# Optimization experiments

Hardware: AMD Instinct MI355X
Metric: run time of the kernel (lower is better)

## Reference

```python
import jax, jax.numpy as jnp
import numpy as np

B, C_IN, C_OUT, T, HID = 8, 32, 32, 8192, 64


def setup_inputs() -> dict:
    key = jax.random.key(0)
    ks = jax.random.split(key, 8)
    s1 = 1.0  # fan_in=1
    s2 = 1.0 / np.sqrt(HID)
    return {
        "x": jax.random.normal(ks[0], (B, C_IN, T), dtype=jnp.float32),
        "w1": jax.random.uniform(ks[1], (1, HID), jnp.float32, -s1, s1),
        "b1": jax.random.uniform(ks[2], (HID,), jnp.float32, -s1, s1),
        "w2": jax.random.uniform(ks[3], (HID, HID), jnp.float32, -s2, s2),
        "b2": jax.random.uniform(ks[4], (HID,), jnp.float32, -s2, s2),
        "w3": jax.random.uniform(ks[5], (HID, C_IN * C_OUT), jnp.float32, -s2, s2),
        "b3": jax.random.uniform(ks[6], (C_IN * C_OUT,), jnp.float32, -s2, s2),
        "bias": jnp.zeros((C_OUT,), dtype=jnp.float32),
    }


def _filters(w1, b1, w2, b2, w3, b3):
    # positions: (T, 1) in [0, 1]
    pos = jnp.linspace(0.0, 1.0, T, dtype=jnp.float32)[:, None]
    h = jax.nn.gelu(pos @ w1 + b1, approximate=False)
    h = jax.nn.gelu(h @ w2 + b2, approximate=False)
    f = h @ w3 + b3                      # (T, out*in)
    f = f.reshape(T, C_OUT, C_IN)
    return jnp.transpose(f, (1, 2, 0))   # (out, in, T)


def reference(x, w1, b1, w2, b2, w3, b3, bias):
    freq_x = jnp.fft.rfft(x, axis=-1)                      # (B, in, F)
    filt = _filters(w1, b1, w2, b2, w3, b3)                # (out, in, T)
    freq_f = jnp.fft.rfft(filt, axis=-1)                   # (out, in, F)
    conv_freq = jnp.einsum('bif,oif->bof', freq_x, freq_f) # contract over in
    out = jnp.fft.irfft(conv_freq, n=T, axis=-1)           # (B, out, T)
    return out + bias[None, :, None]
```

## Files before the change

### kernel.cpp

```cpp
#include <hip/hip_runtime.h>
#include <math.h>

#define T 8192
#define M 4096
#define JS 4104
#define B 8
#define CIN 32
#define COUT 32
#define HID 64
#define FT 4

__device__ inline float2 cadd(float2 a, float2 b){ return make_float2(a.x+b.x, a.y+b.y); }
__device__ inline float2 csub(float2 a, float2 b){ return make_float2(a.x-b.x, a.y-b.y); }
__device__ inline float2 cmul(float2 a, float2 b){ return make_float2(a.x*b.x - a.y*b.y, a.x*b.y + a.y*b.x); }
__device__ inline float2 cmulc(float2 a, float2 b){
    return make_float2(a.x*b.x + a.y*b.y, a.y*b.x - a.x*b.y); }
__device__ inline int swz(int p){ return p ^ ((p >> 5) & 31); }
__device__ inline int brev12(int v){ return (int)(__brev((unsigned)v) >> 20); }

__device__ inline float gelu_exact(float x){
    return 0.5f*x*(1.0f + erff(x*0.70710678118654752440f));
}

template<int S, int SH0>
__device__ inline void dif_group8(float2 q[8], int r, const float2* __restrict__ tw){
    #pragma unroll
    for (int st = 0; st < 3; ++st){
        const int d = 4 >> st;
        const int sh = SH0 + st;
        #pragma unroll
        for (int k = 0; k < 4; ++k){
            const int jd = k & (d-1);
            const int lo = ((k & ~(d-1)) << 1) | jd;
            const int hi = lo + d;
            float2 w = tw[(r + S*jd) << sh];
            float2 a = q[lo], b = q[hi];
            q[lo] = cadd(a, b);
            q[hi] = cmul(csub(a, b), w);
        }
    }
}
template<int S, int SH0>
__device__ inline void dit_group8(float2 q[8], int r, const float2* __restrict__ tw){
    #pragma unroll
    for (int st = 0; st < 3; ++st){
        const int d = 1 << st;
        const int sh = SH0 - st;
        #pragma unroll
        for (int k = 0; k < 4; ++k){
            const int jd = k & (d-1);
            const int lo = ((k & ~(d-1)) << 1) | jd;
            const int hi = lo + d;
            float2 w = tw[(r + S*jd) << sh];
            float2 a = q[lo];
            float2 t2 = cmulc(q[hi], w);
            q[lo] = cadd(a, t2);
            q[hi] = csub(a, t2);
        }
    }
}

__device__ inline void lds_store8(float2* sc, const float2* q, int base, int S){
    #pragma unroll
    for (int l = 0; l < 8; ++l) sc[swz(base + S*l)] = q[l];
}
__device__ inline void lds_load8(const float2* sc, float2* q, int base, int S){
    #pragma unroll
    for (int l = 0; l < 8; ++l) q[l] = sc[swz(base + S*l)];
}

__global__ __launch_bounds__(512) void rfft_all(const float* __restrict__ x,
        const float* __restrict__ H, const float2* __restrict__ tw,
        float2* __restrict__ Xh, float2* __restrict__ Hh){
    __shared__ float2 sc[M];
    const int t = threadIdx.x;
    const int sig = blockIdx.x;
    const float* srow;
    float2* dp;
    if (sig < B*CIN){ srow = x + (size_t)sig*T;        dp = Xh + (size_t)sig*JS; }
    else            { srow = H + (size_t)(sig-B*CIN)*T; dp = Hh + (size_t)(sig-B*CIN)*JS; }
    const float2* zp = (const float2*)srow;
    float2 q[8];
    #pragma unroll
    for (int l = 0; l < 8; ++l) q[l] = zp[t + 512*l];
    dif_group8<512,1>(q, t, tw);
    lds_store8(sc, q, t, 512);
    __syncthreads();
    {
        const int base = ((t>>6)<<9) | (t&63);
        lds_load8(sc, q, base, 64);
        dif_group8<64,4>(q, t&63, tw);
        lds_store8(sc, q, base, 64);
    }
    {
        const int base = ((t>>3)<<6) | (t&7);
        lds_load8(sc, q, base, 8);
        dif_group8<8,7>(q, t&7, tw);
        lds_store8(sc, q, base, 8);
    }
    {
        const int base = t << 3;
        lds_load8(sc, q, base, 1);
        dif_group8<1,10>(q, 0, tw);
        lds_store8(sc, q, base, 1);
    }
    __syncthreads();
    #pragma unroll
    for (int l = 0; l < 8; ++l){
        const int j  = t + 512*l;
        const int k  = brev12(j);
        const int j2 = brev12((M - k) & (M-1));
        float2 Z  = sc[swz(j)];
        float2 Zm = sc[swz(j2)];
        float2 E = make_float2(0.5f*(Z.x + Zm.x), 0.5f*(Z.y - Zm.y));
        float2 D = make_float2(Z.x - Zm.x, Z.y + Zm.y);
        float2 O = make_float2(0.5f*D.y, -0.5f*D.x);
        dp[j] = cadd(E, cmul(tw[k], O));
        if (j == 0) dp[M] = make_float2(Z.x - Z.y, 0.0f);
    }
}

__global__ __launch_bounds__(512) void irfft_out(const float2* __restrict__ Yh,
        const float2* __restrict__ tw, const float* __restrict__ bias, float* __restrict__ out){
    __shared__ float2 sc[M];
    const int t = threadIdx.x;
    const int sig = blockIdx.x;
    const float2* yp = Yh + (size_t)sig*JS;
    #pragma unroll
    for (int l = 0; l < 8; ++l){
        const int j = t + 512*l;
        sc[swz(j)] = yp[j];
    }
    float2 yM = yp[M];
    __syncthreads();
    #pragma unroll
    for (int l = 0; l < 4; ++l){
        const int j = (t + 512*l) << 1;
        const int k = brev12(j);
        float2 Ym; int j2 = 0;
        if (k == 0){ Ym = yM; }
        else { j2 = brev12(M - k); Ym = sc[swz(j2)]; }
        float2 Y = sc[swz(j)];
        float2 E = make_float2(0.5f*(Y.x + Ym.x), 0.5f*(Y.y - Ym.y));
        float2 D = make_float2(0.5f*(Y.x - Ym.x), 0.5f*(Y.y + Ym.y));
        float2 O = cmulc(D, tw[k]);
        sc[swz(j)] = make_float2(E.x - O.y, E.y + O.x);
        if (k != 0){
            sc[swz(j2)] = make_float2(E.x + O.y, O.x - E.y);
        }
    }
    if (t == 0){
        float2 Y = sc[swz(1)];
        float2 E = make_float2(Y.x, 0.0f);
        float2 D = make_float2(0.0f, Y.y);
        float2 O = cmulc(D, tw[2048]);
        sc[swz(1)] = make_float2(E.x - O.y, E.y + O.x);
    }
    __syncthreads();
    float2 q[8];
    {
        const int base = t << 3;
        lds_load8(sc, q, base, 1);
        dit_group8<1,12>(q, 0, tw);
        lds_store8(sc, q, base, 1);
    }
    {
        const int base = ((t>>3)<<6) | (t&7);
        lds_load8(sc, q, base, 8);
        dit_group8<8,9>(q, t&7, tw);
        lds_store8(sc, q, base, 8);
    }
    {
        const int base = ((t>>6)<<9) | (t&63);
        lds_load8(sc, q, base, 64);
        dit_group8<64,6>(q, t&63, tw);
        lds_store8(sc, q, base, 64);
    }
    __syncthreads();
    lds_load8(sc, q, t, 512);
    dit_group8<512,3>(q, t, tw);
    const float scv = 1.0f/(float)M;
    const float bv = bias[sig & (COUT-1)];
    float2* op = (float2*)(out + (size_t)sig*T);
    #pragma unroll
    for (int l = 0; l < 8; ++l)
        op[t + 512*l] = make_float2(q[l].x*scv + bv, q[l].y*scv + bv);
}

#define TB 32
__global__ __launch_bounds__(256) void mlp_hidden(const float* __restrict__ w1, const float* __restrict__ b1,
                           const float* __restrict__ w2, const float* __restrict__ b2,
                           float* __restrict__ H, float2* __restrict__ tw){
    __shared__ float sw1[HID], sb1[HID], sw2[HID*HID], sb2[HID];
    __shared__ float h1s[TB][HID+1];
    const int tid = threadIdx.x;
    if (blockIdx.x < 16){
        const int k = blockIdx.x*256 + tid;
        float ang = -6.28318530717958647692f * (float)k / (float)T;
        float s, c;
        sincosf(ang, &s, &c);
        tw[k] = make_float2(c, s);
    }
    for (int i = tid; i < HID; i += 256){ sw1[i]=w1[i]; sb1[i]=b1[i]; sb2[i]=b2[i]; }
    for (int i = tid; i < HID*HID; i += 256) sw2[i]=w2[i];
    __syncthreads();
    const int t0 = blockIdx.x * TB;
    for (int e = tid; e < TB*HID; e += 256){
        const int tl = e & (TB-1), h = e >> 5;
        const float pos = (float)(t0 + tl) / (float)(T-1);
        h1s[tl][h] = gelu_exact(pos*sw1[h] + sb1[h]);
    }
    __syncthreads();
    const int tl = tid & (TB-1), hg = tid >> 5;
    float acc[8];
    #pragma unroll
    for (int u = 0; u < 8; ++u) acc[u] = sb2[hg*8 + u];
    for (int k = 0; k < HID; ++k){
        const float hv = h1s[tl][k];
        const float4 wa = *(const float4*)&sw2[k*HID + hg*8];
        const float4 wb = *(const float4*)&sw2[k*HID + hg*8 + 4];
        acc[0] += hv*wa.x; acc[1] += hv*wa.y; acc[2] += hv*wa.z; acc[3] += hv*wa.w;
        acc[4] += hv*wb.x; acc[5] += hv*wb.y; acc[6] += hv*wb.z; acc[7] += hv*wb.w;
    }
    #pragma unroll
    for (int u = 0; u < 8; ++u)
        H[(size_t)(hg*8 + u)*T + t0 + tl] = gelu_exact(acc[u]);
}

__global__ __launch_bounds__(256) void filt_contract(const float* __restrict__ w3,
        const float* __restrict__ b3, const float2* __restrict__ Hh,
        const float2* __restrict__ Xh, float2* __restrict__ Yh){
    __shared__ float XsRe[CIN][FT][B+1];
    __shared__ float XsIm[CIN][FT][B+1];
    __shared__ float FltRe[FT][16][33];
    __shared__ float FltIm[FT][16][33];
    const int t = threadIdx.x;
    const int f0 = blockIdx.x * FT;
    const int oh = blockIdx.y;
    {
        const float4* xp4 = (const float4*)(Xh + (size_t)t*JS + f0);
        float4 u0 = xp4[0], u1 = xp4[1];
        const int b = t >> 5, i = t & 31;
        XsRe[i][0][b] = u0.x; XsIm[i][0][b] = u0.y;
        XsRe[i][1][b] = u0.z; XsIm[i][1][b] = u0.w;
        XsRe[i][2][b] = u1.x; XsIm[i][2][b] = u1.y;
        XsRe[i][3][b] = u1.z; XsIm[i][3][b] = u1.w;
    }
    const int oiG = oh*512 + (t << 1);
    float2 acc[2][FT];
    #pragma unroll
    for (int ii = 0; ii < 2; ++ii)
        #pragma unroll
        for (int f = 0; f < FT; ++f) acc[ii][f] = make_float2(0.f, 0.f);
    #pragma unroll 4
    for (int h = 0; h < HID; ++h){
        const float2 w2v = *(const float2*)(w3 + (size_t)h*(CIN*COUT) + oiG);
        const float2* hp = Hh + (size_t)h*JS + f0;
        float2 h0 = hp[0], h1 = hp[1], h2 = hp[2], h3 = hp[3];
        const float wv[2] = {w2v.x, w2v.y};
        #pragma unroll
        for (int ii = 0; ii < 2; ++ii){
            acc[ii][0].x += wv[ii]*h0.x; acc[ii][0].y += wv[ii]*h0.y;
            acc[ii][1].x += wv[ii]*h1.x; acc[ii][1].y += wv[ii]*h1.y;
            acc[ii][2].x += wv[ii]*h2.x; acc[ii][2].y += wv[ii]*h2.y;
            acc[ii][3].x += wv[ii]*h3.x; acc[ii][3].y += wv[ii]*h3.y;
        }
    }
    if (f0 == 0){
        #pragma unroll
        for (int ii = 0; ii < 2; ++ii)
            acc[ii][0].x += (float)T * b3[oiG + ii];
    }
    {
        const int oL = t >> 4;
        const int ib = (t & 15) << 1;
        #pragma unroll
        for (int ii = 0; ii < 2; ++ii)
            #pragma unroll
            for (int f = 0; f < FT; ++f){
                FltRe[f][oL][ib + ii] = acc[ii][f].x;
                FltIm[f][oL][ib + ii] = acc[ii][f].y;
            }
    }
    __syncthreads();
    const int o2 = t >> 4, f2 = (t >> 2) & 3, g = t & 3;
    float2 y[2];
    y[0] = make_float2(0.f, 0.f); y[1] = make_float2(0.f, 0.f);
    #pragma unroll 8
    for (int i0 = 0; i0 < CIN; ++i0){
        const float2 fv = make_float2(FltRe[f2][o2][i0], FltIm[f2][o2][i0]);
        #pragma unroll
        for (int j = 0; j < 2; ++j){
            const int b = (g << 1) | j;
            const float2 xv = make_float2(XsRe[i0][f2][b], XsIm[i0][f2][b]);
            y[j].x += xv.x*fv.x - xv.y*fv.y;
            y[j].y += xv.x*fv.y + xv.y*fv.x;
        }
    }
    if (f0 + f2 <= M){
        #pragma unroll
        for (int j = 0; j < 2; ++j){
            const int b = (g << 1) | j;
            const int o = oh*16 + o2;
            Yh[((size_t)(b*COUT + o))*JS + f0 + f2] = y[j];
        }
    }
}

extern "C" void kernel_launch(void* const* d_in, const int* in_sizes, int n_in,
                              void* d_out, int out_size, void* d_ws, size_t ws_size,
                              hipStream_t stream){
    const float* x    = (const float*)d_in[0];
    const float* w1   = (const float*)d_in[1];
    const float* b1   = (const float*)d_in[2];
    const float* w2   = (const float*)d_in[3];
    const float* b2   = (const float*)d_in[4];
    const float* w3   = (const float*)d_in[5];
    const float* b3   = (const float*)d_in[6];
    const float* bias = (const float*)d_in[7];
    float* out = (float*)d_out;

    char* ws = (char*)d_ws;
    float2* Xh = (float2*)ws;
    float2* Yh = (float2*)(ws + (size_t)9*1024*1024);
    float2* Hh = (float2*)(ws + (size_t)18*1024*1024);
    float*  H  = (float*) (ws + (size_t)21*1024*1024);
    float2* tws= (float2*)(ws + (size_t)23*1024*1024);

    hipLaunchKernelGGL(mlp_hidden,    dim3(T/TB),      dim3(256), 0, stream, w1, b1, w2, b2, H, tws);
    hipLaunchKernelGGL(rfft_all,      dim3(B*CIN+HID), dim3(512), 0, stream, x, H, tws, Xh, Hh);
    hipLaunchKernelGGL(filt_contract, dim3(M/FT + 1, 2), dim3(256), 0, stream, w3, b3, Hh, Xh, Yh);
    hipLaunchKernelGGL(irfft_out,     dim3(B*COUT),    dim3(512), 0, stream, Yh, tws, bias, out);
}
```

Baseline: 143.8 us.

## Split forward and inverse FFTs into two global passes for more blocks

The single-block-per-signal rfft and irfft kernels are each split into two kernels. The first radix-8 stage goes through a global scratch buffer, and the remaining stages run in small 128-thread blocks that each own two 512-element sub-FFTs. The sub-FFTs are paired so each conjugate-symmetric index partner lives in the same block. The aim is many more, smaller blocks, raising occupancy and spreading work across CUs beyond the 320 and 256 blocks used before. In exchange it adds an extra global write and read of the full spectrum plus two more kernel launches.

New measurement: 145.1 us. About the same (+0.9%).

```diff
diff --git a/kernel.cpp b/kernel.cpp
--- a/kernel.cpp
+++ b/kernel.cpp
@@ -15,7 +15,7 @@
 __device__ inline float2 cmul(float2 a, float2 b){ return make_float2(a.x*b.x - a.y*b.y, a.x*b.y + a.y*b.x); }
 __device__ inline float2 cmulc(float2 a, float2 b){
     return make_float2(a.x*b.x + a.y*b.y, a.y*b.x - a.x*b.y); }
-__device__ inline int swz(int p){ return p ^ ((p >> 5) & 31); }
+__device__ inline int swzl(int p){ return p ^ ((p >> 5) & 31); }
 __device__ inline int brev12(int v){ return (int)(__brev((unsigned)v) >> 20); }
 
 __device__ inline float gelu_exact(float x){
@@ -60,58 +60,68 @@
     }
 }
 
-__device__ inline void lds_store8(float2* sc, const float2* q, int base, int S){
-    #pragma unroll
-    for (int l = 0; l < 8; ++l) sc[swz(base + S*l)] = q[l];
-}
-__device__ inline void lds_load8(const float2* sc, float2* q, int base, int S){
-    #pragma unroll
-    for (int l = 0; l < 8; ++l) q[l] = sc[swz(base + S*l)];
-}
-
-__global__ __launch_bounds__(512) void rfft_all(const float* __restrict__ x,
-        const float* __restrict__ H, const float2* __restrict__ tw,
-        float2* __restrict__ Xh, float2* __restrict__ Hh){
-    __shared__ float2 sc[M];
-    const int t = threadIdx.x;
-    const int sig = blockIdx.x;
-    const float* srow;
-    float2* dp;
-    if (sig < B*CIN){ srow = x + (size_t)sig*T;        dp = Xh + (size_t)sig*JS; }
-    else            { srow = H + (size_t)(sig-B*CIN)*T; dp = Hh + (size_t)(sig-B*CIN)*JS; }
+__device__ __constant__ int c0s[4] = {0, 2, 4, 5};
+__device__ __constant__ int c1s[4] = {1, 3, 7, 6};
+
+__global__ __launch_bounds__(256) void fft_pass1(const float* __restrict__ x,
+        const float* __restrict__ H, const float2* __restrict__ tw, float2* __restrict__ W){
+    const int u = blockIdx.x*256 + threadIdx.x;
+    const int sig = u >> 9, tau = u & 511;
+    const float* srow = (sig < B*CIN) ? (x + (size_t)sig*T) : (H + (size_t)(sig - B*CIN)*T);
     const float2* zp = (const float2*)srow;
     float2 q[8];
     #pragma unroll
-    for (int l = 0; l < 8; ++l) q[l] = zp[t + 512*l];
-    dif_group8<512,1>(q, t, tw);
-    lds_store8(sc, q, t, 512);
-    __syncthreads();
-    {
-        const int base = ((t>>6)<<9) | (t&63);
-        lds_load8(sc, q, base, 64);
-        dif_group8<64,4>(q, t&63, tw);
-        lds_store8(sc, q, base, 64);
-    }
-    {
-        const int base = ((t>>3)<<6) | (t&7);
-        lds_load8(sc, q, base, 8);
-        dif_group8<8,7>(q, t&7, tw);
-        lds_store8(sc, q, base, 8);
-    }
-    {
-        const int base = t << 3;
-        lds_load8(sc, q, base, 1);
+    for (int l = 0; l < 8; ++l) q[l] = zp[tau + 512*l];
+    dif_group8<512,1>(q, tau, tw);
+    float2* wp = W + (size_t)sig*M;
+    #pragma unroll
+    for (int l = 0; l < 8; ++l) wp[l*512 + tau] = q[l];
+}
+
+__global__ __launch_bounds__(128) void fft_pass2(const float2* __restrict__ W,
+        const float2* __restrict__ tw, float2* __restrict__ Xh, float2* __restrict__ Hh){
+    __shared__ float2 ld[1024];
+    const int pid = blockIdx.x, sig = blockIdx.y;
+    const int tid = threadIdx.x, w = tid >> 6, r = tid & 63;
+    const int cc0 = c0s[pid], cc1 = c1s[pid];
+    const int c = w ? cc1 : cc0;
+    const int base = w << 9;
+    const float2* wp = W + (size_t)sig*M + c*512;
+    float2 q[8];
+    #pragma unroll
+    for (int l = 0; l < 8; ++l) q[l] = wp[r + 64*l];
+    dif_group8<64,4>(q, r, tw);
+    #pragma unroll
+    for (int l = 0; l < 8; ++l) ld[base + swzl(r + 64*l)] = q[l];
+    {
+        const int b8 = ((r>>3)<<6) | (r&7);
+        #pragma unroll
+        for (int l = 0; l < 8; ++l) q[l] = ld[base + swzl(b8 + 8*l)];
+        dif_group8<8,7>(q, r&7, tw);
+        #pragma unroll
+        for (int l = 0; l < 8; ++l) ld[base + swzl(b8 + 8*l)] = q[l];
+    }
+    {
+        const int b1 = r << 3;
+        #pragma unroll
+        for (int l = 0; l < 8; ++l) q[l] = ld[base + swzl(b1 + l)];
         dif_group8<1,10>(q, 0, tw);
-        lds_store8(sc, q, base, 1);
-    }
-    __syncthreads();
+        #pragma unroll
+        for (int l = 0; l < 8; ++l) ld[base + swzl(b1 + l)] = q[l];
+    }
+    __syncthreads();
+    float2* dp = (sig < B*CIN) ? (Xh + (size_t)sig*JS) : (Hh + (size_t)(sig - B*CIN)*JS);
     #pragma unroll
     for (int l = 0; l < 8; ++l){
-        const int j  = t + 512*l;
+        const int bp = tid + 128*l;
+        const int h  = bp >> 9, p = bp & 511;
+        const int j  = ((h ? cc1 : cc0) << 9) + p;
         const int k  = brev12(j);
         const int j2 = brev12((M - k) & (M-1));
-        float2 Z  = sc[swz(j)];
-        float2 Zm = sc[swz(j2)];
+        const int p2 = j2 & 511;
+        const int h2 = ((j2 >> 9) == cc1) ? 1 : 0;
+        float2 Z  = ld[(h  << 9) + swzl(p)];
+        float2 Zm = ld[(h2 << 9) + swzl(p2)];
         float2 E = make_float2(0.5f*(Z.x + Zm.x), 0.5f*(Z.y - Zm.y));
         float2 D = make_float2(Z.x - Zm.x, Z.y + Zm.y);
         float2 O = make_float2(0.5f*D.y, -0.5f*D.x);
@@ -120,71 +130,93 @@
     }
 }
 
-__global__ __launch_bounds__(512) void irfft_out(const float2* __restrict__ Yh,
-        const float2* __restrict__ tw, const float* __restrict__ bias, float* __restrict__ out){
-    __shared__ float2 sc[M];
-    const int t = threadIdx.x;
-    const int sig = blockIdx.x;
+__global__ __launch_bounds__(128) void ifft_pass1(const float2* __restrict__ Yh,
+        const float2* __restrict__ tw, float2* __restrict__ W2){
+    __shared__ float2 ld[1024];
+    const int pid = blockIdx.x, sig = blockIdx.y;
+    const int tid = threadIdx.x, w = tid >> 6, r = tid & 63;
+    const int cc0 = c0s[pid], cc1 = c1s[pid];
     const float2* yp = Yh + (size_t)sig*JS;
     #pragma unroll
     for (int l = 0; l < 8; ++l){
-        const int j = t + 512*l;
-        sc[swz(j)] = yp[j];
-    }
-    float2 yM = yp[M];
+        const int bp = tid + 128*l;
+        const int h = bp >> 9, p = bp & 511;
+        const int j = ((h ? cc1 : cc0) << 9) + p;
+        ld[(h << 9) + swzl(p)] = yp[j];
+    }
+    const float2 yM = yp[M];
     __syncthreads();
     #pragma unroll
     for (int l = 0; l < 4; ++l){
-        const int j = (t + 512*l) << 1;
+        const int bpe = (tid + 128*l) << 1;
+        const int h = bpe >> 9, p = bpe & 511;
+        const int j = ((h ? cc1 : cc0) << 9) + p;
         const int k = brev12(j);
-        float2 Ym; int j2 = 0;
+        float2 Y = ld[(h << 9) + swzl(p)];
+        float2 Ym; int h2 = 0, p2 = 0;
         if (k == 0){ Ym = yM; }
-        else { j2 = brev12(M - k); Ym = sc[swz(j2)]; }
-        float2 Y = sc[swz(j)];
+        else {
+            const int j2 = brev12(M - k);
+            p2 = j2 & 511;
+            h2 = ((j2 >> 9) == cc1) ? 1 : 0;
+            Ym = ld[(h2 << 9) + swzl(p2)];
+        }
         float2 E = make_float2(0.5f*(Y.x + Ym.x), 0.5f*(Y.y - Ym.y));
         float2 D = make_float2(0.5f*(Y.x - Ym.x), 0.5f*(Y.y + Ym.y));
         float2 O = cmulc(D, tw[k]);
-        sc[swz(j)] = make_float2(E.x - O.y, E.y + O.x);
-        if (k != 0){
-            sc[swz(j2)] = make_float2(E.x + O.y, O.x - E.y);
-        }
-    }
-    if (t == 0){
-        float2 Y = sc[swz(1)];
+        ld[(h << 9) + swzl(p)] = make_float2(E.x - O.y, E.y + O.x);
+        if (k != 0)
+            ld[(h2 << 9) + swzl(p2)] = make_float2(E.x + O.y, O.x - E.y);
+    }
+    if (pid == 0 && tid == 0){
+        float2 Y = ld[swzl(1)];
         float2 E = make_float2(Y.x, 0.0f);
         float2 D = make_float2(0.0f, Y.y);
         float2 O = cmulc(D, tw[2048]);
-        sc[swz(1)] = make_float2(E.x - O.y, E.y + O.x);
-    }
-    __syncthreads();
+        ld[swzl(1)] = make_float2(E.x - O.y, E.y + O.x);
+    }
+    __syncthreads();
+    const int base = w << 9;
     float2 q[8];
     {
-        const int base = t << 3;
-        lds_load8(sc, q, base, 1);
+        const int b1 = r << 3;
+        #pragma unroll
+        for (int l = 0; l < 8; ++l) q[l] = ld[base + swzl(b1 + l)];
         dit_group8<1,12>(q, 0, tw);
-        lds_store8(sc, q, base, 1);
-    }
-    {
-        const int base = ((t>>3)<<6) | (t&7);
-        lds_load8(sc, q, base, 8);
-        dit_group8<8,9>(q, t&7, tw);
-        lds_store8(sc, q, base, 8);
-    }
-    {
-        const int base = ((t>>6)<<9) | (t&63);
-        lds_load8(sc, q, base, 64);
-        dit_group8<64,6>(q, t&63, tw);
-        lds_store8(sc, q, base, 64);
-    }
-    __syncthreads();
-    lds_load8(sc, q, t, 512);
-    dit_group8<512,3>(q, t, tw);
+        #pragma unroll
+        for (int l = 0; l < 8; ++l) ld[base + swzl(b1 + l)] = q[l];
+    }
+    {
+        const int b8 = ((r>>3)<<6) | (r&7);
+        #pragma unroll
+        for (int l = 0; l < 8; ++l) q[l] = ld[base + swzl(b8 + 8*l)];
+        dit_group8<8,9>(q, r&7, tw);
+        #pragma unroll
+        for (int l = 0; l < 8; ++l) ld[base + swzl(b8 + 8*l)] = q[l];
+    }
+    #pragma unroll
+    for (int l = 0; l < 8; ++l) q[l] = ld[base + swzl(r + 64*l)];
+    dit_group8<64,6>(q, r, tw);
+    float2* wp = W2 + (size_t)sig*M + (w ? cc1 : cc0)*512;
+    #pragma unroll
+    for (int l = 0; l < 8; ++l) wp[r + 64*l] = q[l];
+}
+
+__global__ __launch_bounds__(256) void ifft_pass2(const float2* __restrict__ W2,
+        const float2* __restrict__ tw, const float* __restrict__ bias, float* __restrict__ out){
+    const int u = blockIdx.x*256 + threadIdx.x;
+    const int sig = u >> 9, tau = u & 511;
+    const float2* wp = W2 + (size_t)sig*M;
+    float2 q[8];
+    #pragma unroll
+    for (int l = 0; l < 8; ++l) q[l] = wp[tau + 512*l];
+    dit_group8<512,3>(q, tau, tw);
     const float scv = 1.0f/(float)M;
     const float bv = bias[sig & (COUT-1)];
     float2* op = (float2*)(out + (size_t)sig*T);
     #pragma unroll
     for (int l = 0; l < 8; ++l)
-        op[t + 512*l] = make_float2(q[l].x*scv + bv, q[l].y*scv + bv);
+        op[tau + 512*l] = make_float2(q[l].x*scv + bv, q[l].y*scv + bv);
 }
 
 #define TB 32
@@ -326,9 +358,14 @@
     float2* Hh = (float2*)(ws + (size_t)18*1024*1024);
     float*  H  = (float*) (ws + (size_t)21*1024*1024);
     float2* tws= (float2*)(ws + (size_t)23*1024*1024);
-
-    hipLaunchKernelGGL(mlp_hidden,    dim3(T/TB),      dim3(256), 0, stream, w1, b1, w2, b2, H, tws);
-    hipLaunchKernelGGL(rfft_all,      dim3(B*CIN+HID), dim3(512), 0, stream, x, H, tws, Xh, Hh);
+    float2* W  = (float2*)(ws + (size_t)24*1024*1024);
+    float2* W2 = (float2*)(ws + (size_t)35*1024*1024);
+
+    const int NSIG = B*CIN + HID;
+    hipLaunchKernelGGL(mlp_hidden,    dim3(T/TB),        dim3(256), 0, stream, w1, b1, w2, b2, H, tws);
+    hipLaunchKernelGGL(fft_pass1,     dim3(NSIG*2),      dim3(256), 0, stream, x, H, tws, W);
+    hipLaunchKernelGGL(fft_pass2,     dim3(4, NSIG),     dim3(128), 0, stream, W, tws, Xh, Hh);
     hipLaunchKernelGGL(filt_contract, dim3(M/FT + 1, 2), dim3(256), 0, stream, w3, b3, Hh, Xh, Yh);
-    hipLaunchKernelGGL(irfft_out,     dim3(B*COUT),    dim3(512), 0, stream, Yh, tws, bias, out);
-}
+    hipLaunchKernelGGL(ifft_pass1,    dim3(4, B*COUT),   dim3(128), 0, stream, Yh, tws, W2);
+    hipLaunchKernelGGL(ifft_pass2,    dim3(B*COUT*2),    dim3(256), 0, stream, W2, tws, bias, out);
+}
```
